# Optimization experiments

Measured on AMD Instinct MI355X. Metric: run time of the kernel, lower is better.

The kernel has to match this reference:

```python
import jax, jax.numpy as jnp
import numpy as np

DIM = 512
N_HEAD = 4
WIN = (5, 9)

def setup_inputs() -> dict:
    key = jax.random.key(0)
    ks = jax.random.split(key, 9)
    s = DIM ** -0.5
    x = jax.random.normal(ks[0], (1, 8, 60, 108, DIM), jnp.float32)
    Wq = jax.random.normal(ks[1], (DIM, DIM), jnp.float32) * s
    bq = jax.random.normal(ks[2], (DIM,), jnp.float32) * 0.02
    Wk = jax.random.normal(ks[3], (DIM, DIM), jnp.float32) * s
    bk = jax.random.normal(ks[4], (DIM,), jnp.float32) * 0.02
    Wv = jax.random.normal(ks[5], (DIM, DIM), jnp.float32) * s
    bv = jax.random.normal(ks[6], (DIM,), jnp.float32) * 0.02
    Wp = jax.random.normal(ks[7], (DIM, DIM), jnp.float32) * s
    bp = jax.random.normal(ks[8], (DIM,), jnp.float32) * 0.02
    return {"x": x, "Wq": Wq, "bq": bq, "Wk": Wk, "bk": bk,
            "Wv": Wv, "bv": bv, "Wp": Wp, "bp": bp}

def reference(x, Wq, bq, Wk, bk, Wv, bv, Wp, bp):
    b, t, h, w, c = x.shape
    w_h, w_w = WIN
    n_head = N_HEAD
    c_head = c // n_head
    n_wh = -(-h // w_h)
    n_ww = -(-w // w_w)
    new_h, new_w = n_wh * w_h, n_ww * w_w
    pad_b, pad_r = new_h - h, new_w - w
    if pad_b > 0 or pad_r > 0:
        x = jnp.pad(x, ((0, 0), (0, 0), (0, pad_b), (0, pad_r), (0, 0)))
    # torch nn.Linear: y = x @ W.T + b, weight shape (out, in)
    q = jnp.einsum('bthwc,dc->bthwd', x, Wq) + bq
    k = jnp.einsum('bthwc,dc->bthwd', x, Wk) + bk
    v = jnp.einsum('bthwc,dc->bthwd', x, Wv) + bv

    def part(z):
        # (b,t,H,W,c) -> (b, n_windows, n_head, t*w_h*w_w, c_head)
        z = z.reshape(b, t, n_wh, w_h, n_ww, w_w, n_head, c_head)
        z = z.transpose(0, 2, 4, 6, 1, 3, 5, 7)
        return z.reshape(b, n_wh * n_ww, n_head, t * w_h * w_w, c_head)

    qw, kw, vw = part(q), part(k), part(v)
    scale = c_head ** -0.5
    # all (batch, window) attentions batched into one einsum (fused form of the torch double loop)
    scores = jnp.einsum('bwnsc,bwnkc->bwnsk', qw, kw) * scale
    attn = jax.nn.softmax(scores, axis=-1)
    out = jnp.einsum('bwnsk,bwnkc->bwnsc', attn, vw)
    # merge windows back: (b,t,new_h,new_w,c)
    out = out.reshape(b, n_wh, n_ww, n_head, t, w_h, w_w, c_head)
    out = out.transpose(0, 4, 1, 5, 2, 6, 3, 7).reshape(b, t, new_h, new_w, c)
    out = out[:, :, :h, :w, :]
    out = jnp.einsum('bthwc,dc->bthwd', out, Wp) + bp
    return out
```

## Files before the change

### kernel.cpp

```cpp
#include <hip/hip_runtime.h>

typedef _Float16 f16;
typedef _Float16 f16x8 __attribute__((ext_vector_type(8)));
typedef _Float16 f16x4 __attribute__((ext_vector_type(4)));
typedef float f32x4 __attribute__((ext_vector_type(4)));
typedef unsigned int u32;
typedef unsigned int u32x4 __attribute__((ext_vector_type(4)));

#define MFMA16(a, b, c) __builtin_amdgcn_mfma_f32_16x16x32_f16(a, b, c, 0, 0, 0)

__device__ __forceinline__ void async_copy16(f16* lds, const f16* g) {
    __builtin_amdgcn_global_load_lds(
        (const __attribute__((address_space(1))) unsigned int*)g,
        (__attribute__((address_space(3))) unsigned int*)lds,
        16, 0, 0);
}

__global__ __launch_bounds__(256) void prep_kernel(
    const float* __restrict__ Wq, const float* __restrict__ Wk,
    const float* __restrict__ Wv, const float* __restrict__ Wp,
    const float* __restrict__ bq, const float* __restrict__ bk,
    const float* __restrict__ bv,
    f16* __restrict__ Wqkv, f16* __restrict__ Wph, float* __restrict__ bqkv,
    int* __restrict__ tokmap)
{
    int i = blockIdx.x * 256 + threadIdx.x;
    if (i < 786432) {
        int r = i >> 9, c = i & 511;
        const float* src = (r < 512) ? Wq : (r < 1024) ? Wk : Wv;
        Wqkv[i] = (f16)src[(r & 511) * 512 + c];
    } else if (i < 786432 + 262144) {
        int j = i - 786432;
        Wph[j] = (f16)Wp[j];
    } else if (i < 786432 + 262144 + 1536) {
        int j = i - (786432 + 262144);
        bqkv[j] = (j < 512) ? bq[j] : (j < 1024) ? bk[j - 512] : bv[j - 1024];
    } else if (i < 786432 + 262144 + 1536 + 51840) {
        int j = i - (786432 + 262144 + 1536);
        int t_ = j / 6480, rem = j % 6480;
        int hh = rem / 108, ww = rem % 108;
        int win = (hh / 5) * 12 + (ww / 9);
        int s = t_ * 45 + (hh % 5) * 9 + (ww % 9);
        tokmap[j] = win * 1440 + s;
    }
}

__global__ __launch_bounds__(256) void convert_x(
    const float* __restrict__ x, f16* __restrict__ xh)
{
    int i = blockIdx.x * 256 + threadIdx.x;
    f32x4 a = *(const f32x4*)(x + (size_t)i * 8);
    f32x4 b = *(const f32x4*)(x + (size_t)i * 8 + 4);
    f16x8 h = { (f16)a[0], (f16)a[1], (f16)a[2], (f16)a[3],
                (f16)b[0], (f16)b[1], (f16)b[2], (f16)b[3] };
    *(f16x8*)(xh + (size_t)i * 8) = h;
}

__global__ __launch_bounds__(256, 3) void qkv_gemm(
    const f16* __restrict__ Xh, const f16* __restrict__ W,
    const float* __restrict__ bias, const int* __restrict__ tokmap,
    f16* __restrict__ Qp, f16* __restrict__ Kp, f16* __restrict__ Vp)
{
    __shared__ __align__(16) f16 As[3][128 * 32];
    __shared__ __align__(16) f16 Bs[3][128 * 32];
    const int tid = threadIdx.x;
    const int lane = tid & 63, wid = tid >> 6;
    const int g = lane >> 4, l15 = lane & 15;
    const int wr = wid >> 1, wc = wid & 1;

    const int orig = blockIdx.x;
    const int xcd = orig & 7;
    const int wg = (xcd < 4 ? xcd * 608 : 2432 + (xcd - 4) * 607) + (orig >> 3);
    const int bn = wg % 12;
    const int brow = (wg / 12) * 128;

    const f16* Abase = Xh + (size_t)brow * 512;
    const f16* Bbase = W + (size_t)bn * 128 * 512;

    f32x4 acc[4][4] = {};

    #define QKV_STAGE(buf, step)                                              \
        {                                                                     \
            const int k0_ = (step) * 32;                                      \
            _Pragma("unroll")                                                 \
            for (int rr = 0; rr < 2; ++rr) {                                  \
                int idx = rr * 256 + tid;                                     \
                int row = idx >> 2, ch = idx & 3;                             \
                int sch = ch ^ ((row >> 1) & 3);                              \
                async_copy16(&As[buf][idx * 8],                               \
                             Abase + (size_t)row * 512 + k0_ + sch * 8);      \
                async_copy16(&Bs[buf][idx * 8],                               \
                             Bbase + (size_t)row * 512 + k0_ + sch * 8);      \
            }                                                                 \
        }

    QKV_STAGE(0, 0);
    QKV_STAGE(1, 1);

    int cur = 0;
    for (int t = 0; t < 16; ++t) {
        if (t < 15) asm volatile("s_waitcnt vmcnt(4)" ::: "memory");
        else        asm volatile("s_waitcnt vmcnt(0)" ::: "memory");
        __builtin_amdgcn_s_barrier();
        __builtin_amdgcn_sched_barrier(0);
        if (t + 2 < 16) {
            int stg = cur + 2; if (stg >= 3) stg -= 3;
            QKV_STAGE(stg, t + 2);
        }
        f16x8 a[4], b[4];
        #pragma unroll
        for (int m = 0; m < 4; ++m) {
            int arow = wr * 64 + m * 16 + l15;
            int sl = g ^ ((arow >> 1) & 3);
            a[m] = *(const f16x8*)&As[cur][arow * 32 + sl * 8];
        }
        #pragma unroll
        for (int n = 0; n < 4; ++n) {
            int brw = wc * 64 + n * 16 + l15;
            int sl = g ^ ((brw >> 1) & 3);
            b[n] = *(const f16x8*)&Bs[cur][brw * 32 + sl * 8];
        }
        __builtin_amdgcn_s_setprio(1);
        #pragma unroll
        for (int m = 0; m < 4; ++m)
            #pragma unroll
            for (int n = 0; n < 4; ++n)
                acc[m][n] = MFMA16(a[m], b[n], acc[m][n]);
        __builtin_amdgcn_s_setprio(0);
        __builtin_amdgcn_s_barrier();
        cur = (cur == 2) ? 0 : cur + 1;
    }
    #undef QKV_STAGE

    const int which = bn >> 2, head = bn & 3;
    f16* dst = (which == 0) ? Qp : (which == 1) ? Kp : Vp;
    #pragma unroll
    for (int m = 0; m < 4; ++m) {
        #pragma unroll
        for (int j = 0; j < 4; ++j) {
            int gm = brow + wr * 64 + m * 16 + g * 4 + j;
            size_t obase = ((size_t)(tokmap[gm] + head * 360)) * 128;
            #pragma unroll
            for (int n = 0; n < 4; ++n) {
                int cidx = wc * 64 + n * 16 + l15;
                float v = acc[m][n][j] + bias[bn * 128 + cidx];
                dst[obase + cidx] = (f16)v;
            }
        }
    }
}

__global__ __launch_bounds__(256, 2) void attn_kernel(
    const f16* __restrict__ Qp, const f16* __restrict__ Kp,
    const f16* __restrict__ Vp, f16* __restrict__ AO)
{
    __shared__ __align__(16) f16 Kl[64 * 136];
    __shared__ __align__(16) f16 Vt[128 * 72];
    __shared__ __align__(16) f16 Pl[192 * 72];

    const int tid = threadIdx.x;
    const int lane = tid & 63, wid = tid >> 6;
    const int g = lane >> 4, l15 = lane & 15;
    const int wh = blockIdx.x >> 1;
    const int half = blockIdx.x & 1;
    const int win = wh >> 2, head = wh & 3;
    const int base = wh * 46080;
    const int qbase = half * 192 + wid * 48;

    const float SC2 = 0.08838834764831845f * 1.4426950408889634f;

    f16x8 qf[3][4];
    #pragma unroll
    for (int qi = 0; qi < 3; ++qi)
        #pragma unroll
        for (int c4 = 0; c4 < 4; ++c4)
            qf[qi][c4] = *(const f16x8*)(Qp + base + (qbase + qi * 16 + l15) * 128 + c4 * 32 + g * 8);

    f32x4 o[3][8] = {};
    float m_r[3] = { -1e30f, -1e30f, -1e30f };
    float l_r[3] = { 0.f, 0.f, 0.f };

    for (int kt = 0; kt < 6; ++kt) {
        #pragma unroll
        for (int it = 0; it < 4; ++it) {
            int idx = it * 256 + tid;
            int krow = idx >> 4, seg = idx & 15;
            f16x8 kv = *(const f16x8*)(Kp + base + (kt * 64 + krow) * 128 + seg * 8);
            *(f16x8*)&Kl[krow * 136 + seg * 8] = kv;
        }
        #pragma unroll
        for (int it = 0; it < 2; ++it) {
            int i2 = it * 256 + tid;
            int kb = i2 >> 6;
            int chp = (i2 & 63) * 2;
            const u32* Vb = (const u32*)(Vp + base);
            u32 d[8];
            #pragma unroll
            for (int i = 0; i < 8; ++i) {
                int kg = kt * 64 + kb * 8 + i;
                d[i] = (kg < 360) ? Vb[kg * 64 + (chp >> 1)] : 0u;
            }
            u32x4 lo, hi;
            #pragma unroll
            for (int jj = 0; jj < 4; ++jj) {
                lo[jj] = (d[2 * jj] & 0xffffu) | (d[2 * jj + 1] << 16);
                hi[jj] = (d[2 * jj] >> 16) | (d[2 * jj + 1] & 0xffff0000u);
            }
            *(u32x4*)&Vt[chp * 72 + kb * 8] = lo;
            *(u32x4*)&Vt[(chp + 1) * 72 + kb * 8] = hi;
        }
        __syncthreads();

        f32x4 sc[4][3] = {};
        __builtin_amdgcn_s_setprio(1);
        #pragma unroll
        for (int c4 = 0; c4 < 4; ++c4) {
            f16x8 ka[4];
            #pragma unroll
            for (int kf = 0; kf < 4; ++kf)
                ka[kf] = *(const f16x8*)&Kl[(kf * 16 + l15) * 136 + c4 * 32 + g * 8];
            #pragma unroll
            for (int kf = 0; kf < 4; ++kf)
                #pragma unroll
                for (int qi = 0; qi < 3; ++qi)
                    sc[kf][qi] = MFMA16(ka[kf], qf[qi][c4], sc[kf][qi]);
        }
        __builtin_amdgcn_s_setprio(0);
        if (kt == 5) {
            #pragma unroll
            for (int kf = 0; kf < 4; ++kf)
                #pragma unroll
                for (int j = 0; j < 4; ++j)
                    if (320 + kf * 16 + g * 4 + j >= 360) {
                        #pragma unroll
                        for (int qi = 0; qi < 3; ++qi) sc[kf][qi][j] = -1e30f;
                    }
        }

        #pragma unroll
        for (int qi = 0; qi < 3; ++qi) {
            float mx = -1e30f;
            #pragma unroll
            for (int kf = 0; kf < 4; ++kf)
                #pragma unroll
                for (int j = 0; j < 4; ++j)
                    mx = fmaxf(mx, sc[kf][qi][j]);
            mx = fmaxf(mx, __shfl_xor(mx, 16));
            mx = fmaxf(mx, __shfl_xor(mx, 32));
            float mnew = fmaxf(m_r[qi], mx);
            float r = exp2f((m_r[qi] - mnew) * SC2);
            m_r[qi] = mnew;
            float psum = 0.f;
            #pragma unroll
            for (int kf = 0; kf < 4; ++kf) {
                f16x4 pv;
                #pragma unroll
                for (int j = 0; j < 4; ++j) {
                    float p = exp2f((sc[kf][qi][j] - mnew) * SC2);
                    psum += p;
                    pv[j] = (f16)p;
                }
                *(f16x4*)&Pl[(wid * 48 + qi * 16 + l15) * 72 + kf * 16 + g * 4] = pv;
            }
            psum += __shfl_xor(psum, 16);
            psum += __shfl_xor(psum, 32);
            l_r[qi] = l_r[qi] * r + psum;
            #pragma unroll
            for (int j = 0; j < 4; ++j) {
                float rj = __shfl(r, g * 4 + j);
                #pragma unroll
                for (int chf = 0; chf < 8; ++chf)
                    o[qi][chf][j] *= rj;
            }
        }

        __builtin_amdgcn_s_setprio(1);
        #pragma unroll
        for (int kc = 0; kc < 2; ++kc) {
            f16x8 pa[3], vb[8];
            #pragma unroll
            for (int qi = 0; qi < 3; ++qi)
                pa[qi] = *(const f16x8*)&Pl[(wid * 48 + qi * 16 + l15) * 72 + kc * 32 + g * 8];
            #pragma unroll
            for (int chf = 0; chf < 8; ++chf)
                vb[chf] = *(const f16x8*)&Vt[(chf * 16 + l15) * 72 + kc * 32 + g * 8];
            #pragma unroll
            for (int qi = 0; qi < 3; ++qi)
                #pragma unroll
                for (int chf = 0; chf < 8; ++chf)
                    o[qi][chf] = MFMA16(pa[qi], vb[chf], o[qi][chf]);
        }
        __builtin_amdgcn_s_setprio(0);
        __syncthreads();
    }

    #pragma unroll
    for (int qi = 0; qi < 3; ++qi) {
        #pragma unroll
        for (int j = 0; j < 4; ++j) {
            float lj = __shfl(l_r[qi], g * 4 + j);
            float inv = 1.0f / lj;
            int s = qbase + qi * 16 + g * 4 + j;
            if (s < 360) {
                int t_ = s / 45, s45 = s % 45;
                int hh = (win / 12) * 5 + s45 / 9;
                int ww = (win % 12) * 9 + s45 % 9;
                int mm = t_ * 6480 + hh * 108 + ww;
                #pragma unroll
                for (int chf = 0; chf < 8; ++chf) {
                    int col = head * 128 + chf * 16 + l15;
                    AO[(size_t)mm * 512 + col] = (f16)(o[qi][chf][j] * inv);
                }
            }
        }
    }
}

__global__ __launch_bounds__(256, 3) void proj_gemm(
    const f16* __restrict__ A, const f16* __restrict__ W,
    const float* __restrict__ bias, float* __restrict__ out)
{
    __shared__ __align__(16) f16 As[3][128 * 32];
    __shared__ __align__(16) f16 Bs[3][128 * 32];
    const int tid = threadIdx.x;
    const int lane = tid & 63, wid = tid >> 6;
    const int g = lane >> 4, l15 = lane & 15;
    const int wr = wid >> 1, wc = wid & 1;

    const int orig = blockIdx.x;
    const int xcd = orig & 7;
    const int wg = (xcd < 4 ? xcd * 203 : 812 + (xcd - 4) * 202) + (orig >> 3);
    const int bcol = (wg & 3) * 128;
    const int brow = (wg >> 2) * 128;

    const f16* Abase = A + (size_t)brow * 512;
    const f16* Bbase = W + (size_t)bcol * 512;

    f32x4 acc[4][4] = {};

    #define PROJ_STAGE(buf, step)                                             \
        {                                                                     \
            const int k0_ = (step) * 32;                                      \
            _Pragma("unroll")                                                 \
            for (int rr = 0; rr < 2; ++rr) {                                  \
                int idx = rr * 256 + tid;                                     \
                int row = idx >> 2, ch = idx & 3;                             \
                int sch = ch ^ ((row >> 1) & 3);                              \
                async_copy16(&As[buf][idx * 8],                               \
                             Abase + (size_t)row * 512 + k0_ + sch * 8);      \
                async_copy16(&Bs[buf][idx * 8],                               \
                             Bbase + (size_t)row * 512 + k0_ + sch * 8);      \
            }                                                                 \
        }

    PROJ_STAGE(0, 0);
    PROJ_STAGE(1, 1);

    int cur = 0;
    for (int t = 0; t < 16; ++t) {
        if (t < 15) asm volatile("s_waitcnt vmcnt(4)" ::: "memory");
        else        asm volatile("s_waitcnt vmcnt(0)" ::: "memory");
        __builtin_amdgcn_s_barrier();
        __builtin_amdgcn_sched_barrier(0);
        if (t + 2 < 16) {
            int stg = cur + 2; if (stg >= 3) stg -= 3;
            PROJ_STAGE(stg, t + 2);
        }
        f16x8 a[4], b[4];
        #pragma unroll
        for (int m = 0; m < 4; ++m) {
            int arow = wr * 64 + m * 16 + l15;
            int sl = g ^ ((arow >> 1) & 3);
            a[m] = *(const f16x8*)&As[cur][arow * 32 + sl * 8];
        }
        #pragma unroll
        for (int n = 0; n < 4; ++n) {
            int brw = wc * 64 + n * 16 + l15;
            int sl = g ^ ((brw >> 1) & 3);
            b[n] = *(const f16x8*)&Bs[cur][brw * 32 + sl * 8];
        }
        __builtin_amdgcn_s_setprio(1);
        #pragma unroll
        for (int m = 0; m < 4; ++m)
            #pragma unroll
            for (int n = 0; n < 4; ++n)
                acc[m][n] = MFMA16(a[m], b[n], acc[m][n]);
        __builtin_amdgcn_s_setprio(0);
        __builtin_amdgcn_s_barrier();
        cur = (cur == 2) ? 0 : cur + 1;
    }
    #undef PROJ_STAGE

    #pragma unroll
    for (int m = 0; m < 4; ++m)
        #pragma unroll
        for (int j = 0; j < 4; ++j) {
            int gm = brow + wr * 64 + m * 16 + g * 4 + j;
            #pragma unroll
            for (int n = 0; n < 4; ++n) {
                int gn = bcol + wc * 64 + n * 16 + l15;
                out[(size_t)gm * 512 + gn] = acc[m][n][j] + bias[gn];
            }
        }
}

extern "C" void kernel_launch(void* const* d_in, const int* in_sizes, int n_in,
                              void* d_out, int out_size, void* d_ws, size_t ws_size,
                              hipStream_t stream)
{
    (void)in_sizes; (void)n_in; (void)out_size; (void)ws_size;
    const float* x  = (const float*)d_in[0];
    const float* Wq = (const float*)d_in[1];
    const float* bq = (const float*)d_in[2];
    const float* Wk = (const float*)d_in[3];
    const float* bk = (const float*)d_in[4];
    const float* Wv = (const float*)d_in[5];
    const float* bv = (const float*)d_in[6];
    const float* Wp = (const float*)d_in[7];
    const float* bp = (const float*)d_in[8];

    f16* Qp   = (f16*)d_ws;
    f16* Kp   = Qp + 26542080;
    f16* Vp   = Kp + 26542080;
    f16* AO   = Vp + 26542080;
    f16* xh   = AO;
    f16* Wqkv = AO + 26542080;
    f16* Wph  = Wqkv + 786432;
    float* bqkv = (float*)(Wph + 262144);
    int* tokmap = (int*)(bqkv + 1536);

    prep_kernel<<<4305, 256, 0, stream>>>(Wq, Wk, Wv, Wp, bq, bk, bv, Wqkv, Wph, bqkv, tokmap);
    convert_x<<<12960, 256, 0, stream>>>(x, xh);
    qkv_gemm<<<4860, 256, 0, stream>>>(xh, Wqkv, bqkv, tokmap, Qp, Kp, Vp);
    attn_kernel<<<1152, 256, 0, stream>>>(Qp, Kp, Vp, AO);
    proj_gemm<<<1620, 256, 0, stream>>>(AO, Wph, bp, (float*)d_out);
}
```

Baseline: 288.3 us.

## Double-buffer K tiles with async LDS copies and XOR swizzle in attention

The attention kernel now stages K tiles straight into a double-buffered LDS array with global_load_lds. The next tile is prefetched while the current tile's MFMAs run, and an XOR swizzle replaces row padding to avoid bank conflicts. The V transpose is reorganised so each thread writes one transposed row. That doubles the per-thread global V reads, some of which are redundant. The __syncthreads calls become raw s_barrier plus an lgkmcnt wait, so correctness relies on the compiler's vmcnt waits for the V loads also covering the async K copies. LDS use grows.

```diff
diff --git a/kernel.cpp b/kernel.cpp
--- a/kernel.cpp
+++ b/kernel.cpp
@@ -154,7 +154,7 @@
     const f16* __restrict__ Qp, const f16* __restrict__ Kp,
     const f16* __restrict__ Vp, f16* __restrict__ AO)
 {
-    __shared__ __align__(16) f16 Kl[64 * 136];
+    __shared__ __align__(16) f16 Kl[2][64 * 128];
     __shared__ __align__(16) f16 Vt[128 * 72];
     __shared__ __align__(16) f16 Pl[192 * 72];
 
@@ -168,6 +168,19 @@
     const int qbase = half * 192 + wid * 48;
 
     const float SC2 = 0.08838834764831845f * 1.4426950408889634f;
+    const u32* Vb = (const u32*)(Vp + base);
+
+    #define STAGE_K(buf, kt_)                                                 \
+        {                                                                     \
+            _Pragma("unroll")                                                 \
+            for (int it = 0; it < 4; ++it) {                                  \
+                int chunk = it * 256 + tid;                                   \
+                int krow = chunk >> 4, c = chunk & 15;                        \
+                int sc_ = c ^ (krow & 7);                                     \
+                async_copy16(&Kl[buf][chunk * 8],                             \
+                    Kp + base + (size_t)((kt_) * 64 + krow) * 128 + sc_ * 8); \
+            }                                                                 \
+        }
 
     f16x8 qf[3][4];
     #pragma unroll
@@ -176,40 +189,35 @@
         for (int c4 = 0; c4 < 4; ++c4)
             qf[qi][c4] = *(const f16x8*)(Qp + base + (qbase + qi * 16 + l15) * 128 + c4 * 32 + g * 8);
 
+    STAGE_K(0, 0);
+
     f32x4 o[3][8] = {};
     float m_r[3] = { -1e30f, -1e30f, -1e30f };
     float l_r[3] = { 0.f, 0.f, 0.f };
 
     for (int kt = 0; kt < 6; ++kt) {
+        const int cb = kt & 1;
         #pragma unroll
         for (int it = 0; it < 4; ++it) {
-            int idx = it * 256 + tid;
-            int krow = idx >> 4, seg = idx & 15;
-            f16x8 kv = *(const f16x8*)(Kp + base + (kt * 64 + krow) * 128 + seg * 8);
-            *(f16x8*)&Kl[krow * 136 + seg * 8] = kv;
-        }
-        #pragma unroll
-        for (int it = 0; it < 2; ++it) {
-            int i2 = it * 256 + tid;
-            int kb = i2 >> 6;
-            int chp = (i2 & 63) * 2;
-            const u32* Vb = (const u32*)(Vp + base);
+            int item = it * 256 + tid;
+            int chp = item & 127;
+            int kb = item >> 7;
             u32 d[8];
             #pragma unroll
             for (int i = 0; i < 8; ++i) {
                 int kg = kt * 64 + kb * 8 + i;
                 d[i] = (kg < 360) ? Vb[kg * 64 + (chp >> 1)] : 0u;
             }
-            u32x4 lo, hi;
-            #pragma unroll
-            for (int jj = 0; jj < 4; ++jj) {
-                lo[jj] = (d[2 * jj] & 0xffffu) | (d[2 * jj + 1] << 16);
-                hi[jj] = (d[2 * jj] >> 16) | (d[2 * jj + 1] & 0xffff0000u);
-            }
-            *(u32x4*)&Vt[chp * 72 + kb * 8] = lo;
-            *(u32x4*)&Vt[(chp + 1) * 72 + kb * 8] = hi;
-        }
-        __syncthreads();
+            u32x4 w;
+            #pragma unroll
+            for (int j = 0; j < 4; ++j)
+                w[j] = (chp & 1) ? ((d[2 * j] >> 16) | (d[2 * j + 1] & 0xffff0000u))
+                                 : ((d[2 * j] & 0xffffu) | (d[2 * j + 1] << 16));
+            *(u32x4*)&Vt[chp * 72 + kb * 8] = w;
+        }
+        asm volatile("s_waitcnt lgkmcnt(0)" ::: "memory");
+        __builtin_amdgcn_s_barrier();
+        if (kt + 1 < 6) STAGE_K(cb ^ 1, kt + 1);
 
         f32x4 sc[4][3] = {};
         __builtin_amdgcn_s_setprio(1);
@@ -217,8 +225,11 @@
         for (int c4 = 0; c4 < 4; ++c4) {
             f16x8 ka[4];
             #pragma unroll
-            for (int kf = 0; kf < 4; ++kf)
-                ka[kf] = *(const f16x8*)&Kl[(kf * 16 + l15) * 136 + c4 * 32 + g * 8];
+            for (int kf = 0; kf < 4; ++kf) {
+                int row = kf * 16 + l15;
+                int sl = (c4 * 4 + g) ^ (row & 7);
+                ka[kf] = *(const f16x8*)&Kl[cb][row * 128 + sl * 8];
+            }
             #pragma unroll
             for (int kf = 0; kf < 4; ++kf)
                 #pragma unroll
@@ -291,8 +302,9 @@
                     o[qi][chf] = MFMA16(pa[qi], vb[chf], o[qi][chf]);
         }
         __builtin_amdgcn_s_setprio(0);
-        __syncthreads();
-    }
+        __builtin_amdgcn_s_barrier();
+    }
+    #undef STAGE_K
 
     #pragma unroll
     for (int qi = 0; qi < 3; ++qi) {
```

After: 332.7 us. 1.15x slower.

## Load GEMM weight fragments directly into registers instead of staging through LDS

Applied to the files above, without the earlier changes.

In both the QKV and projection GEMMs, the weight (B) tiles are no longer copied asynchronously into shared memory. Each wave now loads its B fragments straight from global memory into double-buffered registers one k-step ahead, while A stays in the triple-buffered LDS pipeline. The goal is to halve LDS footprint and remove the B-side LDS traffic and its share of the barrier-gated staging. In exchange, each weight element is fetched by two waves from global memory or cache, register pressure rises, and the hand-written vmcnt waits and fully unrolled loop become more fragile.

```diff
diff --git a/kernel.cpp b/kernel.cpp
--- a/kernel.cpp
+++ b/kernel.cpp
@@ -62,7 +62,6 @@
     f16* __restrict__ Qp, f16* __restrict__ Kp, f16* __restrict__ Vp)
 {
     __shared__ __align__(16) f16 As[3][128 * 32];
-    __shared__ __align__(16) f16 Bs[3][128 * 32];
     const int tid = threadIdx.x;
     const int lane = tid & 63, wid = tid >> 6;
     const int g = lane >> 4, l15 = lane & 15;
@@ -75,11 +74,11 @@
     const int brow = (wg / 12) * 128;
 
     const f16* Abase = Xh + (size_t)brow * 512;
-    const f16* Bbase = W + (size_t)bn * 128 * 512;
+    const f16* Bl = W + (size_t)(bn * 128 + wc * 64 + l15) * 512 + g * 8;
 
     f32x4 acc[4][4] = {};
 
-    #define QKV_STAGE(buf, step)                                              \
+    #define STAGE_A(buf, step)                                                \
         {                                                                     \
             const int k0_ = (step) * 32;                                      \
             _Pragma("unroll")                                                 \
@@ -89,48 +88,58 @@
                 int sch = ch ^ ((row >> 1) & 3);                              \
                 async_copy16(&As[buf][idx * 8],                               \
                              Abase + (size_t)row * 512 + k0_ + sch * 8);      \
-                async_copy16(&Bs[buf][idx * 8],                               \
-                             Bbase + (size_t)row * 512 + k0_ + sch * 8);      \
-            }                                                                 \
-        }
-
-    QKV_STAGE(0, 0);
-    QKV_STAGE(1, 1);
+            }                                                                 \
+        }
+
+    #define LOAD_B(dstarr, step)                                              \
+        {                                                                     \
+            _Pragma("unroll")                                                 \
+            for (int n_ = 0; n_ < 4; ++n_)                                    \
+                dstarr[n_] = *(const f16x8*)(Bl + n_ * 8192 + (step) * 32);   \
+        }
+
+    #define GEMM_STEP(t_, BC, BN_)                                            \
+        {                                                                     \
+            asm volatile("s_waitcnt vmcnt(6)" ::: "memory");                  \
+            __builtin_amdgcn_s_barrier();                                     \
+            __builtin_amdgcn_sched_barrier(0);                                \
+            if ((t_) + 2 < 16) {                                              \
+                int stg = cur + 2; if (stg >= 3) stg -= 3;                    \
+                STAGE_A(stg, (t_) + 2);                                       \
+            }                                                                 \
+            if ((t_) + 1 < 16) LOAD_B(BN_, (t_) + 1);                         \
+            f16x8 a[4];                                                       \
+            _Pragma("unroll")                                                 \
+            for (int m_ = 0; m_ < 4; ++m_) {                                  \
+                int arow = wr * 64 + m_ * 16 + l15;                           \
+                int sl = g ^ ((arow >> 1) & 3);                               \
+                a[m_] = *(const f16x8*)&As[cur][arow * 32 + sl * 8];          \
+            }                                                                 \
+            __builtin_amdgcn_s_setprio(1);                                    \
+            _Pragma("unroll")                                                 \
+            for (int m_ = 0; m_ < 4; ++m_)                                    \
+                _Pragma("unroll")                                             \
+                for (int n_ = 0; n_ < 4; ++n_)                                \
+                    acc[m_][n_] = MFMA16(a[m_], BC[n_], acc[m_][n_]);         \
+            __builtin_amdgcn_s_setprio(0);                                    \
+            __builtin_amdgcn_s_barrier();                                     \
+            cur = (cur == 2) ? 0 : cur + 1;                                   \
+        }
+
+    f16x8 b0[4], b1[4];
+    STAGE_A(0, 0);
+    STAGE_A(1, 1);
+    LOAD_B(b0, 0);
 
     int cur = 0;
-    for (int t = 0; t < 16; ++t) {
-        if (t < 15) asm volatile("s_waitcnt vmcnt(4)" ::: "memory");
-        else        asm volatile("s_waitcnt vmcnt(0)" ::: "memory");
-        __builtin_amdgcn_s_barrier();
-        __builtin_amdgcn_sched_barrier(0);
-        if (t + 2 < 16) {
-            int stg = cur + 2; if (stg >= 3) stg -= 3;
-            QKV_STAGE(stg, t + 2);
-        }
-        f16x8 a[4], b[4];
-        #pragma unroll
-        for (int m = 0; m < 4; ++m) {
-            int arow = wr * 64 + m * 16 + l15;
-            int sl = g ^ ((arow >> 1) & 3);
-            a[m] = *(const f16x8*)&As[cur][arow * 32 + sl * 8];
-        }
-        #pragma unroll
-        for (int n = 0; n < 4; ++n) {
-            int brw = wc * 64 + n * 16 + l15;
-            int sl = g ^ ((brw >> 1) & 3);
-            b[n] = *(const f16x8*)&Bs[cur][brw * 32 + sl * 8];
-        }
-        __builtin_amdgcn_s_setprio(1);
-        #pragma unroll
-        for (int m = 0; m < 4; ++m)
-            #pragma unroll
-            for (int n = 0; n < 4; ++n)
-                acc[m][n] = MFMA16(a[m], b[n], acc[m][n]);
-        __builtin_amdgcn_s_setprio(0);
-        __builtin_amdgcn_s_barrier();
-        cur = (cur == 2) ? 0 : cur + 1;
-    }
-    #undef QKV_STAGE
+    #pragma unroll
+    for (int tt = 0; tt < 8; ++tt) {
+        GEMM_STEP(2 * tt,     b0, b1);
+        GEMM_STEP(2 * tt + 1, b1, b0);
+    }
+    #undef GEMM_STEP
+    #undef LOAD_B
+    #undef STAGE_A
 
     const int which = bn >> 2, head = bn & 3;
     f16* dst = (which == 0) ? Qp : (which == 1) ? Kp : Vp;
@@ -321,7 +330,6 @@
     const float* __restrict__ bias, float* __restrict__ out)
 {
     __shared__ __align__(16) f16 As[3][128 * 32];
-    __shared__ __align__(16) f16 Bs[3][128 * 32];
     const int tid = threadIdx.x;
     const int lane = tid & 63, wid = tid >> 6;
     const int g = lane >> 4, l15 = lane & 15;
@@ -334,11 +342,11 @@
     const int brow = (wg >> 2) * 128;
 
     const f16* Abase = A + (size_t)brow * 512;
-    const f16* Bbase = W + (size_t)bcol * 512;
+    const f16* Bl = W + (size_t)(bcol + wc * 64 + l15) * 512 + g * 8;
 
     f32x4 acc[4][4] = {};
 
-    #define PROJ_STAGE(buf, step)                                             \
+    #define STAGE_A(buf, step)                                                \
         {                                                                     \
             const int k0_ = (step) * 32;                                      \
             _Pragma("unroll")                                                 \
@@ -348,48 +356,58 @@
                 int sch = ch ^ ((row >> 1) & 3);                              \
                 async_copy16(&As[buf][idx * 8],                               \
                              Abase + (size_t)row * 512 + k0_ + sch * 8);      \
-                async_copy16(&Bs[buf][idx * 8],                               \
-                             Bbase + (size_t)row * 512 + k0_ + sch * 8);      \
-            }                                                                 \
-        }
-
-    PROJ_STAGE(0, 0);
-    PROJ_STAGE(1, 1);
+            }                                                                 \
+        }
+
+    #define LOAD_B(dstarr, step)                                              \
+        {                                                                     \
+            _Pragma("unroll")                                                 \
+            for (int n_ = 0; n_ < 4; ++n_)                                    \
+                dstarr[n_] = *(const f16x8*)(Bl + n_ * 8192 + (step) * 32);   \
+        }
+
+    #define GEMM_STEP(t_, BC, BN_)                                            \
+        {                                                                     \
+            asm volatile("s_waitcnt vmcnt(6)" ::: "memory");                  \
+            __builtin_amdgcn_s_barrier();                                     \
+            __builtin_amdgcn_sched_barrier(0);                                \
+            if ((t_) + 2 < 16) {                                              \
+                int stg = cur + 2; if (stg >= 3) stg -= 3;                    \
+                STAGE_A(stg, (t_) + 2);                                       \
+            }                                                                 \
+            if ((t_) + 1 < 16) LOAD_B(BN_, (t_) + 1);                         \
+            f16x8 a[4];                                                       \
+            _Pragma("unroll")                                                 \
+            for (int m_ = 0; m_ < 4; ++m_) {                                  \
+                int arow = wr * 64 + m_ * 16 + l15;                           \
+                int sl = g ^ ((arow >> 1) & 3);                               \
+                a[m_] = *(const f16x8*)&As[cur][arow * 32 + sl * 8];          \
+            }                                                                 \
+            __builtin_amdgcn_s_setprio(1);                                    \
+            _Pragma("unroll")                                                 \
+            for (int m_ = 0; m_ < 4; ++m_)                                    \
+                _Pragma("unroll")                                             \
+                for (int n_ = 0; n_ < 4; ++n_)                                \
+                    acc[m_][n_] = MFMA16(a[m_], BC[n_], acc[m_][n_]);         \
+            __builtin_amdgcn_s_setprio(0);                                    \
+            __builtin_amdgcn_s_barrier();                                     \
+            cur = (cur == 2) ? 0 : cur + 1;                                   \
+        }
+
+    f16x8 b0[4], b1[4];
+    STAGE_A(0, 0);
+    STAGE_A(1, 1);
+    LOAD_B(b0, 0);
 
     int cur = 0;
-    for (int t = 0; t < 16; ++t) {
-        if (t < 15) asm volatile("s_waitcnt vmcnt(4)" ::: "memory");
-        else        asm volatile("s_waitcnt vmcnt(0)" ::: "memory");
-        __builtin_amdgcn_s_barrier();
-        __builtin_amdgcn_sched_barrier(0);
-        if (t + 2 < 16) {
-            int stg = cur + 2; if (stg >= 3) stg -= 3;
-            PROJ_STAGE(stg, t + 2);
-        }
-        f16x8 a[4], b[4];
-        #pragma unroll
-        for (int m = 0; m < 4; ++m) {
-            int arow = wr * 64 + m * 16 + l15;
-            int sl = g ^ ((arow >> 1) & 3);
-            a[m] = *(const f16x8*)&As[cur][arow * 32 + sl * 8];
-        }
-        #pragma unroll
-        for (int n = 0; n < 4; ++n) {
-            int brw = wc * 64 + n * 16 + l15;
-            int sl = g ^ ((brw >> 1) & 3);
-            b[n] = *(const f16x8*)&Bs[cur][brw * 32 + sl * 8];
-        }
-        __builtin_amdgcn_s_setprio(1);
-        #pragma unroll
-        for (int m = 0; m < 4; ++m)
-            #pragma unroll
-            for (int n = 0; n < 4; ++n)
-                acc[m][n] = MFMA16(a[m], b[n], acc[m][n]);
-        __builtin_amdgcn_s_setprio(0);
-        __builtin_amdgcn_s_barrier();
-        cur = (cur == 2) ? 0 : cur + 1;
-    }
-    #undef PROJ_STAGE
+    #pragma unroll
+    for (int tt = 0; tt < 8; ++tt) {
+        GEMM_STEP(2 * tt,     b0, b1);
+        GEMM_STEP(2 * tt + 1, b1, b0);
+    }
+    #undef GEMM_STEP
+    #undef LOAD_B
+    #undef STAGE_A
 
     #pragma unroll
     for (int m = 0; m < 4; ++m)
```

Result: slower. 379.7 us (+31.7%).
